# Optimization experiments

Hardware: AMD Instinct MI355X
Metric: run time of the kernel (lower is better)

Reference implementation:

```python
import jax, jax.numpy as jnp
from jax import lax
import numpy as np

TEMPERATURE = 100.0
UNROLL = 1000
N = 2048


def setup_inputs() -> dict:
    key = jax.random.key(0)
    # kaiming_uniform_(a=sqrt(5)) on an NxN matrix -> U(-b, b) with b = sqrt(6/((1+5)*N)) = 1/sqrt(N)
    bound = 1.0 / np.sqrt(N)
    matrix = jax.random.uniform(key, (N, N), dtype=jnp.float32, minval=-bound, maxval=bound)
    return {"matrix": matrix}


def reference(matrix):
    n = matrix.shape[0]
    # numerically-shifted exponential: exp(T * (M - rowmax))
    m = jnp.exp(TEMPERATURE * (matrix - jnp.max(matrix, axis=1, keepdims=True)))

    def sinkhorn_step(m, _):
        m = m / jnp.sum(m, axis=1, keepdims=True)  # row normalize
        m = m / jnp.sum(m, axis=0, keepdims=True)  # col normalize
        return m, None

    m, _ = lax.scan(sinkhorn_step, m, None, length=UNROLL)

    lower = jnp.tril(jnp.ones((n, n), dtype=matrix.dtype))
    # output_lower = (M @ L @ M^T)^T
    output_lower = (m @ lower @ m.T).T
    return output_lower
```

## Files before the change

### kernel.cpp

```cpp
#include <hip/hip_runtime.h>

#define NN 2048
#define ITERS 1000
#define NBLK 256
#define RPW 8
#define EPS 3e-3f

typedef __attribute__((ext_vector_type(4))) float floatx4;
typedef unsigned long long u64;

#define AGENT __HIP_MEMORY_SCOPE_AGENT

static __device__ __forceinline__ void agstore64(u64* p, u64 v) {
  __hip_atomic_store(p, v, __ATOMIC_RELAXED, AGENT);
}
static __device__ __forceinline__ u64 agload64(const u64* p) {
  return __hip_atomic_load(p, __ATOMIC_RELAXED, AGENT);
}
static __device__ __forceinline__ u64 pack(float f, unsigned tag) {
  return ((u64)tag << 32) | (u64)__float_as_uint(f);
}

static __device__ __forceinline__ void poll8(const u64* rec, int tid,
                                             unsigned tag, float* x) {
  const u64* base = rec + tid * 8;
  unsigned got = 0;
  while (got != 0xFFu) {
#pragma unroll
    for (int j = 0; j < 8; j++)
      if (!(got & (1u << j))) {
        u64 wv = agload64(base + j);
        if ((unsigned)(wv >> 32) == tag) {
          x[j] = __uint_as_float((unsigned)wv);
          got |= 1u << j;
        }
      }
  }
}

static __device__ __forceinline__ void gather64(const u64* rec, int tid,
                                                float* vec, unsigned tag) {
  float x[8];
  poll8(rec, tid, tag, x);
#pragma unroll
  for (int j = 0; j < 8; j++) vec[tid * 8 + j] = x[j];
  __syncthreads();
}

static __device__ __forceinline__ bool gather64_check(const u64* rec, int tid,
                                                      float* vec, unsigned tag,
                                                      float* pv) {
  float x[8];
  poll8(rec, tid, tag, x);
  float resid = 0.f;
#pragma unroll
  for (int j = 0; j < 8; j++) {
    resid = fmaxf(resid, fabsf(x[j] / pv[j] - 1.0f));
    pv[j] = x[j];
    vec[tid * 8 + j] = x[j];
  }
  return __syncthreads_and(resid < EPS) != 0;
}

__global__ __launch_bounds__(256) void sinkhorn_kernel(
    const float* __restrict__ M, u64* recU, u64* recV,
    unsigned char* __restrict__ Pb, unsigned char* __restrict__ Wb)
{
  __shared__ float rowsA[RPW][NN];
  __shared__ float colsA[RPW][NN];
  __shared__ float vec[NN];
  __shared__ float myu[RPW];

  const int g = blockIdx.x;
  const int tid = threadIdx.x;
  const int w = tid >> 6;
  const int lane = tid & 63;
  const int r0 = 2 * w, r1 = r0 + 1;

  {
    const float4* src = (const float4*)(M + (size_t)g * RPW * NN);
    float4* dst = (float4*)&rowsA[0][0];
    for (int c = tid; c < RPW * NN / 4; c += 256) {
      float4 x = src[c];
      x.x = __expf(100.0f * x.x);
      x.y = __expf(100.0f * x.y);
      x.z = __expf(100.0f * x.z);
      x.w = __expf(100.0f * x.w);
      dst[c] = x;
    }
  }

  float4 sx0[8], sx1[8];
#pragma unroll
  for (int rr = 0; rr < 8; rr++) {
    const float* src = M + (size_t)(tid * 8 + rr) * NN + RPW * g;
    sx0[rr] = *(const float4*)src;
    sx1[rr] = *(const float4*)(src + 4);
  }

  __syncthreads();

  float s0 = 0.f, s1 = 0.f;
#pragma unroll 8
  for (int k = lane; k < NN; k += 64) {
    s0 += rowsA[r0][k];
    s1 += rowsA[r1][k];
  }
  for (int off = 32; off; off >>= 1) {
    s0 += __shfl_xor(s0, off, 64);
    s1 += __shfl_xor(s1, off, 64);
  }
  {
    float u0 = 1.0f / s0, u1 = 1.0f / s1;
    if (lane == 0) {
      agstore64(&recU[RPW * g + r0], pack(u0, 2));
      agstore64(&recU[RPW * g + r1], pack(u1, 2));
      myu[r0] = u0;
      myu[r1] = u1;
    }
  }

#pragma unroll
  for (int rr = 0; rr < 8; rr++) {
    int i = tid * 8 + rr;
    colsA[0][i] = __expf(100.0f * sx0[rr].x);
    colsA[1][i] = __expf(100.0f * sx0[rr].y);
    colsA[2][i] = __expf(100.0f * sx0[rr].z);
    colsA[3][i] = __expf(100.0f * sx0[rr].w);
    colsA[4][i] = __expf(100.0f * sx1[rr].x);
    colsA[5][i] = __expf(100.0f * sx1[rr].y);
    colsA[6][i] = __expf(100.0f * sx1[rr].z);
    colsA[7][i] = __expf(100.0f * sx1[rr].w);
  }

  float pv[8];
#pragma unroll
  for (int j = 0; j < 8; j++) pv[j] = 1.0f;

  gather64(recU, tid, vec, 2);
  {
    float t0 = 0.f, t1 = 0.f;
#pragma unroll 8
    for (int k = lane; k < NN; k += 64) {
      float uu = vec[k];
      t0 += colsA[r0][k] * uu;
      t1 += colsA[r1][k] * uu;
    }
    for (int off = 32; off; off >>= 1) {
      t0 += __shfl_xor(t0, off, 64);
      t1 += __shfl_xor(t1, off, 64);
    }
    if (lane == 0) {
      agstore64(&recV[RPW * g + r0], pack(1.0f / t0, 3));
      agstore64(&recV[RPW * g + r1], pack(1.0f / t1, 3));
    }
  }

  bool done = false;
  unsigned utag = 4;
  for (int it = 1; it < ITERS; it++, utag += 2) {
    if (gather64_check(recV, tid, vec, utag - 1, pv)) { done = true; break; }
    float a0 = 0.f, a1 = 0.f;
#pragma unroll 8
    for (int k = lane; k < NN; k += 64) {
      float vv = vec[k];
      a0 += rowsA[r0][k] * vv;
      a1 += rowsA[r1][k] * vv;
    }
    for (int off = 32; off; off >>= 1) {
      a0 += __shfl_xor(a0, off, 64);
      a1 += __shfl_xor(a1, off, 64);
    }
    {
      float u0 = 1.0f / a0, u1 = 1.0f / a1;
      if (lane == 0) {
        agstore64(&recU[RPW * g + r0], pack(u0, utag));
        agstore64(&recU[RPW * g + r1], pack(u1, utag));
        myu[r0] = u0;
        myu[r1] = u1;
      }
    }

    gather64(recU, tid, vec, utag);
    float t0 = 0.f, t1 = 0.f;
#pragma unroll 8
    for (int k = lane; k < NN; k += 64) {
      float uu = vec[k];
      t0 += colsA[r0][k] * uu;
      t1 += colsA[r1][k] * uu;
    }
    for (int off = 32; off; off >>= 1) {
      t0 += __shfl_xor(t0, off, 64);
      t1 += __shfl_xor(t1, off, 64);
    }
    if (lane == 0) {
      agstore64(&recV[RPW * g + r0], pack(1.0f / t0, utag + 1));
      agstore64(&recV[RPW * g + r1], pack(1.0f / t1, utag + 1));
    }
  }
  if (!done) gather64(recV, tid, vec, 2 * ITERS + 1);

  for (int idx = tid; idx < RPW * NN / 2; idx += 256) {
    int r = idx >> 10, j2 = (idx & 1023) * 2;
    float p0 = 256.0f * myu[r] * rowsA[r][j2] * vec[j2];
    float p1 = 256.0f * myu[r] * rowsA[r][j2 + 1] * vec[j2 + 1];
    int pk = __builtin_amdgcn_cvt_pk_fp8_f32(p0, p1, 0, false);
    ((unsigned short*)Pb)[((((size_t)(RPW * g + r)) << 11) | j2) >> 1] = (unsigned short)pk;
  }
  for (int rr = 0; rr < 2; rr++) {
    int r = 2 * w + rr;
    float ur = myu[r];
    int base = lane * 32;
    float cs = 0.f;
    for (int t = 0; t < 32; t++) {
      int k = base + ((t + lane) & 31);
      cs += ur * rowsA[r][k] * vec[k];
    }
    float s = cs;
    for (int off = 1; off < 64; off <<= 1) {
      float t = __shfl_down(s, off, 64);
      if (lane + off < 64) s += t;
    }
    float run = __shfl_down(s, 1, 64);
    if (lane == 63) run = 0.f;
    float wv[32];
#pragma unroll
    for (int k = 31; k >= 0; k--) {
      int kk = base + k;
      run += ur * rowsA[r][kk] * vec[kk];
      wv[k] = run;
    }
#pragma unroll
    for (int pq = 0; pq < 16; pq++) {
      int pk = __builtin_amdgcn_cvt_pk_fp8_f32(wv[2 * pq], wv[2 * pq + 1], 0, false);
      ((unsigned short*)Wb)[((((size_t)(RPW * g + r)) << 11) | (base + 2 * pq)) >> 1] =
          (unsigned short)pk;
    }
  }
}

__global__ __launch_bounds__(256, 3) void gemm_nt_fp8(const unsigned char* __restrict__ P,
                                                      const unsigned char* __restrict__ W,
                                                      float* __restrict__ out)
{
  __shared__ unsigned char SA[3][16384];
  const int tid = threadIdx.x;
  const int w = tid >> 6, lane = tid & 63;
  const int quad = lane >> 4, l16 = lane & 15;
  const int i0 = blockIdx.y * 128, j0 = blockIdx.x * 128;
  const int wr = (w >> 1) * 64;
  const int wc = (w & 1) * 64;

  const int lrow = lane >> 2;
  const int lp2 = (lane & 3) * 2;

  floatx4 acc[4][4] = {};

  auto issue = [&](int k0, int b) {
#pragma unroll
    for (int c = 0; c < 4; c++) {
      int q = w * 4 + c;
      int r = q * 16 + lrow;
      const unsigned char* gsrc =
          (q < 8 ? P + (size_t)(i0 + r) * NN
                 : W + (size_t)(j0 + r - 128) * NN) +
          k0 + ((lp2 ^ (r & 6)) * 8);
      __builtin_amdgcn_global_load_lds(
          (const __attribute__((address_space(1))) void*)gsrc,
          (__attribute__((address_space(3))) void*)(&SA[b][q * 1024]), 16, 0, 0);
    }
  };

  issue(0, 0);
  issue(64, 1);
  issue(128, 2);

  for (int k0 = 0; k0 < NN; k0 += 64) {
    const int b = (k0 >> 6) % 3;
    if (k0 + 128 < NN) {
      __builtin_amdgcn_s_waitcnt(0x0F78);
    } else if (k0 + 64 < NN) {
      __builtin_amdgcn_s_waitcnt(0x0F74);
    } else {
      __builtin_amdgcn_s_waitcnt(0x0F70);
    }
    asm volatile("" ::: "memory");
    __builtin_amdgcn_s_barrier();
    asm volatile("" ::: "memory");

#pragma unroll
    for (int kc = 0; kc < 2; kc++) {
      long a[4], b2[4];
      int cg = kc * 4 + quad;
#pragma unroll
      for (int mt = 0; mt < 4; mt++) {
        int r = wr + mt * 16 + l16;
        a[mt] = *(const long*)(&SA[b][r * 64 + ((cg ^ (r & 6)) * 8)]);
      }
#pragma unroll
      for (int nt = 0; nt < 4; nt++) {
        int r = 128 + wc + nt * 16 + l16;
        b2[nt] = *(const long*)(&SA[b][r * 64 + ((cg ^ (r & 6)) * 8)]);
      }
#pragma unroll
      for (int mt = 0; mt < 4; mt++)
#pragma unroll
        for (int nt = 0; nt < 4; nt++)
          acc[mt][nt] = __builtin_amdgcn_mfma_f32_16x16x32_fp8_fp8(a[mt], b2[nt], acc[mt][nt], 0, 0, 0);
    }

    if (k0 + 192 < NN) {
      __builtin_amdgcn_s_waitcnt(0xC07F);
      asm volatile("" ::: "memory");
      __builtin_amdgcn_s_barrier();
      asm volatile("" ::: "memory");
      issue(k0 + 192, b);
    }
  }

#pragma unroll
  for (int mt = 0; mt < 4; mt++)
#pragma unroll
    for (int nt = 0; nt < 4; nt++)
#pragma unroll
      for (int e = 0; e < 4; e++) {
        int row = i0 + wr + mt * 16 + quad * 4 + e;
        int col = j0 + wc + nt * 16 + l16;
        out[(size_t)row * NN + col] = acc[mt][nt][e] * 0.00390625f;
      }
}

extern "C" void kernel_launch(void* const* d_in, const int* in_sizes, int n_in,
                              void* d_out, int out_size, void* d_ws, size_t ws_size,
                              hipStream_t stream) {
  const float* M = (const float*)d_in[0];
  float* out = (float*)d_out;
  char* ws = (char*)d_ws;

  u64* recU = (u64*)(ws + 4096);
  u64* recV = (u64*)(ws + 20480);
  unsigned char* Pb = (unsigned char*)(ws + (1u << 20));
  unsigned char* Wb = (unsigned char*)(ws + (1u << 20) + (8u << 20));

  hipMemsetAsync(ws + 4096, 0, 32768, stream);

  sinkhorn_kernel<<<dim3(NBLK), dim3(256), 0, stream>>>(M, recU, recV, Pb, Wb);
  gemm_nt_fp8<<<dim3(16, 16), dim3(256), 0, stream>>>(Pb, Wb, out);
}
```

Baseline: 134.0 us.

## Deepen FP8 GEMM LDS prefetch pipeline to eight stages at one block per CU

Result: no change. 134.1 us (+0.1%).

```diff
diff --git a/kernel.cpp b/kernel.cpp
--- a/kernel.cpp
+++ b/kernel.cpp
@@ -10,6 +10,10 @@
 typedef unsigned long long u64;
 
 #define AGENT __HIP_MEMORY_SCOPE_AGENT
+
+#define WC_VM28  0x4F7C
+#define WC_VM0   0x0F70
+#define WC_LGKM0 0xC07F
 
 static __device__ __forceinline__ void agstore64(u64* p, u64 v) {
   __hip_atomic_store(p, v, __ATOMIC_RELAXED, AGENT);
@@ -239,11 +243,11 @@
   }
 }
 
-__global__ __launch_bounds__(256, 3) void gemm_nt_fp8(const unsigned char* __restrict__ P,
+__global__ __launch_bounds__(256, 1) void gemm_nt_fp8(const unsigned char* __restrict__ P,
                                                       const unsigned char* __restrict__ W,
                                                       float* __restrict__ out)
 {
-  __shared__ unsigned char SA[3][16384];
+  __shared__ unsigned char SA[8][16384];
   const int tid = threadIdx.x;
   const int w = tid >> 6, lane = tid & 63;
   const int quad = lane >> 4, l16 = lane & 15;
@@ -271,52 +275,54 @@
     }
   };
 
-  issue(0, 0);
-  issue(64, 1);
-  issue(128, 2);
-
-  for (int k0 = 0; k0 < NN; k0 += 64) {
-    const int b = (k0 >> 6) % 3;
-    if (k0 + 128 < NN) {
-      __builtin_amdgcn_s_waitcnt(0x0F78);
-    } else if (k0 + 64 < NN) {
-      __builtin_amdgcn_s_waitcnt(0x0F74);
-    } else {
-      __builtin_amdgcn_s_waitcnt(0x0F70);
-    }
+  auto consume = [&](int b) {
+#pragma unroll
+    for (int kc = 0; kc < 2; kc++) {
+      long a[4], b2[4];
+      int cg = kc * 4 + quad;
+#pragma unroll
+      for (int mt = 0; mt < 4; mt++) {
+        int r = wr + mt * 16 + l16;
+        a[mt] = *(const long*)(&SA[b][r * 64 + ((cg ^ (r & 6)) * 8)]);
+      }
+#pragma unroll
+      for (int nt = 0; nt < 4; nt++) {
+        int r = 128 + wc + nt * 16 + l16;
+        b2[nt] = *(const long*)(&SA[b][r * 64 + ((cg ^ (r & 6)) * 8)]);
+      }
+#pragma unroll
+      for (int mt = 0; mt < 4; mt++)
+#pragma unroll
+        for (int nt = 0; nt < 4; nt++)
+          acc[mt][nt] = __builtin_amdgcn_mfma_f32_16x16x32_fp8_fp8(a[mt], b2[nt], acc[mt][nt], 0, 0, 0);
+    }
+  };
+
+#pragma unroll
+  for (int s = 0; s < 8; s++) issue(s * 64, s);
+
+#pragma unroll 1
+  for (int i = 0; i < 24; i++) {
+    __builtin_amdgcn_s_waitcnt(WC_VM28);
     asm volatile("" ::: "memory");
     __builtin_amdgcn_s_barrier();
     asm volatile("" ::: "memory");
 
-#pragma unroll
-    for (int kc = 0; kc < 2; kc++) {
-      long a[4], b2[4];
-      int cg = kc * 4 + quad;
-#pragma unroll
-      for (int mt = 0; mt < 4; mt++) {
-        int r = wr + mt * 16 + l16;
-        a[mt] = *(const long*)(&SA[b][r * 64 + ((cg ^ (r & 6)) * 8)]);
-      }
-#pragma unroll
-      for (int nt = 0; nt < 4; nt++) {
-        int r = 128 + wc + nt * 16 + l16;
-        b2[nt] = *(const long*)(&SA[b][r * 64 + ((cg ^ (r & 6)) * 8)]);
-      }
-#pragma unroll
-      for (int mt = 0; mt < 4; mt++)
-#pragma unroll
-        for (int nt = 0; nt < 4; nt++)
-          acc[mt][nt] = __builtin_amdgcn_mfma_f32_16x16x32_fp8_fp8(a[mt], b2[nt], acc[mt][nt], 0, 0, 0);
-    }
-
-    if (k0 + 192 < NN) {
-      __builtin_amdgcn_s_waitcnt(0xC07F);
-      asm volatile("" ::: "memory");
-      __builtin_amdgcn_s_barrier();
-      asm volatile("" ::: "memory");
-      issue(k0 + 192, b);
-    }
-  }
+    consume(i & 7);
+
+    __builtin_amdgcn_s_waitcnt(WC_LGKM0);
+    asm volatile("" ::: "memory");
+    __builtin_amdgcn_s_barrier();
+    asm volatile("" ::: "memory");
+    issue((i + 8) * 64, i & 7);
+  }
+
+  __builtin_amdgcn_s_waitcnt(WC_VM0);
+  asm volatile("" ::: "memory");
+  __builtin_amdgcn_s_barrier();
+  asm volatile("" ::: "memory");
+#pragma unroll 1
+  for (int i = 24; i < 32; i++) consume(i & 7);
 
 #pragma unroll
   for (int mt = 0; mt < 4; mt++)
```
